# Kernel optimization log

Measured on AMD Instinct MI355X. Metric: run time of the kernel, lower is better.

## Reference

```python
import jax, jax.numpy as jnp
import numpy as np

NUM_HEADS = 64
D_K = 8  # n_wires of the quantum circuit


def setup_inputs() -> dict:
    key = jax.random.key(0)
    k1, k2, k3 = jax.random.split(key, 3)
    B, S, E = 8, 8192, NUM_HEADS * D_K
    x = jax.random.normal(k1, (B, S, E), dtype=jnp.float32)
    # trainable RX rotation angles, one per wire, shared across heads
    theta = jax.random.normal(k2, (D_K,), dtype=jnp.float32)
    # out_proj weight (torch nn.Linear stores [out_features, in_features]); bias=False
    W_out = jax.random.normal(k3, (E, E), dtype=jnp.float32) * 0.02
    return {"x": x, "theta": theta, "W_out": W_out}


def reference(x, theta, W_out):
    B, S, E = x.shape
    H, d = NUM_HEADS, D_K
    # Quantum circuit per (batch, seq, head) element:
    # RX(x_i) then RX(theta_i) on wire i from |0>, <Z_i> = cos(x_i + theta_i).
    xr = x.reshape(B, S, H, d)               # (B, S, H, d_k)
    A = jnp.cos(xr + theta)                  # broadcast theta over wires
    # torch stacks heads first -> (B, H, S, d), then .view(B, S, E) on the
    # contiguous buffer (a memory-layout reinterpretation, not a head-merge).
    A = jnp.transpose(A, (0, 2, 1, 3)).reshape(B, S, E)
    # out_proj: y = A @ W^T (no bias)
    return A @ W_out.T
```

## Files before the change

### kernel.cpp

```cpp
#include <hip/hip_runtime.h>
#include <hip/hip_bf16.h>

typedef __attribute__((ext_vector_type(8))) short short8;
typedef __attribute__((ext_vector_type(4))) float float4v;
typedef __attribute__((ext_vector_type(4))) unsigned int uint4v;
typedef __attribute__((ext_vector_type(2))) unsigned int uint2v;

#define SS 8192
#define EE 512
#define NKB 16
#define AP 520

__device__ __forceinline__ unsigned int f2bf1(float f) {
    unsigned int u = __builtin_bit_cast(unsigned int, f);
    return (u + 0x7fffu + ((u >> 16) & 1u)) >> 16;
}
__device__ __forceinline__ unsigned int pack2(float lo, float hi) {
    return f2bf1(lo) | (f2bf1(hi) << 16);
}

__global__ void w_prep(const float* __restrict__ W, unsigned short* __restrict__ Wws) {
    int idx = blockIdx.x * 256 + threadIdx.x;
    int n  = idx >> 7;
    int kg = idx & 127;
    int k  = kg * 4;
    float4v v = *(const float4v*)(W + (size_t)n * EE + k);
    int kb = k >> 5, kl = k & 31;
    unsigned short* dst = Wws + ((size_t)kb * (EE * 32) + (size_t)n * 32 + kl);
    uint2v pk = { pack2(v.x, v.y), pack2(v.z, v.w) };
    *(uint2v*)dst = pk;
}

__global__ __launch_bounds__(256, 2)
void qmha_fused5(const float* __restrict__ x, const float* __restrict__ theta,
                 const unsigned short* __restrict__ Wws, float* __restrict__ out)
{
    __shared__ __attribute__((aligned(16))) unsigned short A_lds[64 * AP];

    const int bx = blockIdx.x;
    const int b  = bx >> 7;
    const int sc = bx & 127;
    const int t = threadIdx.x, lane = t & 63, wid = t >> 6;
    const int fr = lane & 15, q = lane >> 4;

    const unsigned short* wbase = Wws + ((size_t)(wid * 128 + fr) * 32 + q * 8);

    short8 bA[8], bB[8];
    #pragma unroll
    for (int nt = 0; nt < 8; ++nt)
        bA[nt] = *(const short8*)(wbase + nt * 512);

    const float th0 = theta[0], th1 = theta[1], th2 = theta[2], th3 = theta[3];
    const float th4 = theta[4], th5 = theta[5], th6 = theta[6], th7 = theta[7];

    {
        const float* xb = x + ((size_t)b * SS + (size_t)sc * 64 + (size_t)wid * 16) * EE + lane * 8;
        unsigned short* aw = A_lds + lane * AP + wid * 128;
        #pragma unroll
        for (int it = 0; it < 16; ++it) {
            const float* px = xb + (size_t)it * EE;
            float4v v0 = *(const float4v*)(px);
            float4v v1 = *(const float4v*)(px + 4);
            float c0 = __cosf(v0.x + th0), c1 = __cosf(v0.y + th1);
            float c2 = __cosf(v0.z + th2), c3 = __cosf(v0.w + th3);
            float c4 = __cosf(v1.x + th4), c5 = __cosf(v1.y + th5);
            float c6 = __cosf(v1.z + th6), c7 = __cosf(v1.w + th7);
            uint4v pk = { pack2(c0,c1), pack2(c2,c3), pack2(c4,c5), pack2(c6,c7) };
            *(uint4v*)(aw + it * 8) = pk;
        }
    }

    __syncthreads();

    float4v acc[4][8];
    #pragma unroll
    for (int i = 0; i < 4; ++i)
        #pragma unroll
        for (int j = 0; j < 8; ++j)
            acc[i][j] = (float4v){0.f, 0.f, 0.f, 0.f};

    const int aoff = fr * AP + q * 8;

    #pragma unroll
    for (int kb = 0; kb < NKB; kb += 2) {
        {
            const unsigned short* wn = wbase + (size_t)(kb + 1) * (EE * 32);
            #pragma unroll
            for (int nt = 0; nt < 8; ++nt)
                bB[nt] = *(const short8*)(wn + nt * 512);
        }
        {
            short8 af[4];
            #pragma unroll
            for (int mt = 0; mt < 4; ++mt)
                af[mt] = *(const short8*)&A_lds[aoff + mt * 16 * AP + kb * 32];
            __builtin_amdgcn_s_setprio(1);
            #pragma unroll
            for (int nt = 0; nt < 8; ++nt)
                #pragma unroll
                for (int mt = 0; mt < 4; ++mt)
                    acc[mt][nt] = __builtin_amdgcn_mfma_f32_16x16x32_bf16(af[mt], bA[nt], acc[mt][nt], 0, 0, 0);
            __builtin_amdgcn_s_setprio(0);
        }
        if (kb + 2 < NKB) {
            const unsigned short* wn = wbase + (size_t)(kb + 2) * (EE * 32);
            #pragma unroll
            for (int nt = 0; nt < 8; ++nt)
                bA[nt] = *(const short8*)(wn + nt * 512);
        }
        {
            short8 af[4];
            #pragma unroll
            for (int mt = 0; mt < 4; ++mt)
                af[mt] = *(const short8*)&A_lds[aoff + mt * 16 * AP + (kb + 1) * 32];
            __builtin_amdgcn_s_setprio(1);
            #pragma unroll
            for (int nt = 0; nt < 8; ++nt)
                #pragma unroll
                for (int mt = 0; mt < 4; ++mt)
                    acc[mt][nt] = __builtin_amdgcn_mfma_f32_16x16x32_bf16(af[mt], bB[nt], acc[mt][nt], 0, 0, 0);
            __builtin_amdgcn_s_setprio(0);
        }
    }

    float* outb = out + (size_t)b * (SS * EE) + (size_t)sc * EE + wid * 128 + fr;
    #pragma unroll
    for (int mt = 0; mt < 4; ++mt) {
        #pragma unroll
        for (int r = 0; r < 4; ++r) {
            const int m = mt * 16 + q * 4 + r;
            float* po = outb + (size_t)m * (128 * EE);
            #pragma unroll
            for (int nt = 0; nt < 8; ++nt)
                po[nt * 16] = acc[mt][nt][r];
        }
    }
}

#define AS 520
#define WSF 40
#define HH 64
__global__ __launch_bounds__(256, 2)
void qmha_fused_fb(const float* __restrict__ x, const float* __restrict__ theta,
                   const float* __restrict__ W, float* __restrict__ out)
{
    __shared__ __attribute__((aligned(16))) unsigned short A_lds[HH * AS];
    __shared__ __attribute__((aligned(16))) unsigned short W_lds[128 * WSF];
    const int bx = blockIdx.x;
    const int ntile = (bx >> 3) & 3;
    const int p = ((bx >> 5) << 3) | (bx & 7);
    const int b = p >> 7;
    const int sc = p & 127;
    const int t = threadIdx.x, lane = t & 63, wid = t >> 6;
    const int wn = t >> 1, wk = (t & 1) * 16;
    const float* Wbase = W + (size_t)(ntile * 128 + wn) * EE + wk;
    float4v wv0 = *(const float4v*)(Wbase + 0);
    float4v wv1 = *(const float4v*)(Wbase + 4);
    float4v wv2 = *(const float4v*)(Wbase + 8);
    float4v wv3 = *(const float4v*)(Wbase + 12);
    const float th0 = theta[0], th1 = theta[1], th2 = theta[2], th3 = theta[3];
    const float th4 = theta[4], th5 = theta[5], th6 = theta[6], th7 = theta[7];
    {
        const float* xb = x + ((size_t)b * SS + (size_t)sc * 64) * EE + lane * 8;
        #pragma unroll
        for (int it = 0; it < 16; ++it) {
            const int s_loc = wid * 16 + it;
            const float* px = xb + (size_t)s_loc * EE;
            float4v v0 = *(const float4v*)(px);
            float4v v1 = *(const float4v*)(px + 4);
            float c0 = __cosf(v0.x + th0), c1 = __cosf(v0.y + th1);
            float c2 = __cosf(v0.z + th2), c3 = __cosf(v0.w + th3);
            float c4 = __cosf(v1.x + th4), c5 = __cosf(v1.y + th5);
            float c6 = __cosf(v1.z + th6), c7 = __cosf(v1.w + th7);
            uint4v pk = { pack2(c0,c1), pack2(c2,c3), pack2(c4,c5), pack2(c6,c7) };
            *(uint4v*)&A_lds[lane * AS + s_loc * 8] = pk;
        }
    }
    float4v acc[2][4];
    #pragma unroll
    for (int i = 0; i < 2; ++i)
        #pragma unroll
        for (int j = 0; j < 4; ++j)
            acc[i][j] = (float4v){0.f, 0.f, 0.f, 0.f};
    const int m0 = (wid >> 1) * 32, n0l = (wid & 1) * 64;
    const int fr = lane & 15, q = lane >> 4;
    const unsigned short* Arow0 = &A_lds[(m0 + fr) * AS + q * 8];
    const unsigned short* Arow1 = Arow0 + 16 * AS;
    const unsigned short* Wrow  = &W_lds[(n0l + fr) * WSF + q * 8];
    for (int kb = 0; kb < NKB; ++kb) {
        __syncthreads();
        {
            uint4v lo = { pack2(wv0.x, wv0.y), pack2(wv0.z, wv0.w),
                          pack2(wv1.x, wv1.y), pack2(wv1.z, wv1.w) };
            uint4v hi = { pack2(wv2.x, wv2.y), pack2(wv2.z, wv2.w),
                          pack2(wv3.x, wv3.y), pack2(wv3.z, wv3.w) };
            *(uint4v*)&W_lds[wn * WSF + wk]     = lo;
            *(uint4v*)&W_lds[wn * WSF + wk + 8] = hi;
        }
        if (kb < NKB - 1) {
            const float* Wn = Wbase + (size_t)(kb + 1) * 32;
            wv0 = *(const float4v*)(Wn + 0);
            wv1 = *(const float4v*)(Wn + 4);
            wv2 = *(const float4v*)(Wn + 8);
            wv3 = *(const float4v*)(Wn + 12);
        }
        __syncthreads();
        short8 a0 = *(const short8*)(Arow0 + kb * 32);
        short8 a1 = *(const short8*)(Arow1 + kb * 32);
        short8 b0 = *(const short8*)(Wrow + 0 * 16 * WSF);
        short8 b1 = *(const short8*)(Wrow + 1 * 16 * WSF);
        short8 b2 = *(const short8*)(Wrow + 2 * 16 * WSF);
        short8 b3 = *(const short8*)(Wrow + 3 * 16 * WSF);
        acc[0][0] = __builtin_amdgcn_mfma_f32_16x16x32_bf16(a0, b0, acc[0][0], 0, 0, 0);
        acc[0][1] = __builtin_amdgcn_mfma_f32_16x16x32_bf16(a0, b1, acc[0][1], 0, 0, 0);
        acc[0][2] = __builtin_amdgcn_mfma_f32_16x16x32_bf16(a0, b2, acc[0][2], 0, 0, 0);
        acc[0][3] = __builtin_amdgcn_mfma_f32_16x16x32_bf16(a0, b3, acc[0][3], 0, 0, 0);
        acc[1][0] = __builtin_amdgcn_mfma_f32_16x16x32_bf16(a1, b0, acc[1][0], 0, 0, 0);
        acc[1][1] = __builtin_amdgcn_mfma_f32_16x16x32_bf16(a1, b1, acc[1][1], 0, 0, 0);
        acc[1][2] = __builtin_amdgcn_mfma_f32_16x16x32_bf16(a1, b2, acc[1][2], 0, 0, 0);
        acc[1][3] = __builtin_amdgcn_mfma_f32_16x16x32_bf16(a1, b3, acc[1][3], 0, 0, 0);
    }
    const int colbase = ntile * 128 + n0l + fr;
    #pragma unroll
    for (int mt = 0; mt < 2; ++mt) {
        #pragma unroll
        for (int r = 0; r < 4; ++r) {
            const int hrow = m0 + mt * 16 + q * 4 + r;
            float* po = out + ((size_t)b * SS + (size_t)hrow * 128 + sc) * EE + colbase;
            po[0 * 16] = acc[mt][0][r];
            po[1 * 16] = acc[mt][1][r];
            po[2 * 16] = acc[mt][2][r];
            po[3 * 16] = acc[mt][3][r];
        }
    }
}

extern "C" void kernel_launch(void* const* d_in, const int* in_sizes, int n_in,
                              void* d_out, int out_size, void* d_ws, size_t ws_size,
                              hipStream_t stream) {
    const float* x     = (const float*)d_in[0];
    const float* theta = (const float*)d_in[1];
    const float* W     = (const float*)d_in[2];
    float* out         = (float*)d_out;

    if (ws_size >= (size_t)EE * EE * sizeof(unsigned short)) {
        unsigned short* Wws = (unsigned short*)d_ws;
        w_prep<<<dim3(256), dim3(256), 0, stream>>>(W, Wws);
        qmha_fused5<<<dim3(1024), dim3(256), 0, stream>>>(x, theta, Wws, out);
    } else {
        qmha_fused_fb<<<dim3(4096), dim3(256), 0, stream>>>(x, theta, W, out);
    }
}
```

Before: 257.7 us.

## Stage A-tile cosine production in chunks and overlap with MFMA loop

```diff
diff --git a/kernel.cpp b/kernel.cpp
--- a/kernel.cpp
+++ b/kernel.cpp
@@ -18,6 +18,8 @@
 __device__ __forceinline__ unsigned int pack2(float lo, float hi) {
     return f2bf1(lo) | (f2bf1(hi) << 16);
 }
+
+#define WAITL()  asm volatile("s_waitcnt lgkmcnt(0)" ::: "memory")
 
 __global__ void w_prep(const float* __restrict__ W, unsigned short* __restrict__ Wws) {
     int idx = blockIdx.x * 256 + threadIdx.x;
@@ -32,7 +34,7 @@
 }
 
 __global__ __launch_bounds__(256, 2)
-void qmha_fused5(const float* __restrict__ x, const float* __restrict__ theta,
+void qmha_fused6(const float* __restrict__ x, const float* __restrict__ theta,
                  const unsigned short* __restrict__ Wws, float* __restrict__ out)
 {
     __shared__ __attribute__((aligned(16))) unsigned short A_lds[64 * AP];
@@ -45,32 +47,55 @@
 
     const unsigned short* wbase = Wws + ((size_t)(wid * 128 + fr) * 32 + q * 8);
 
-    short8 bA[8], bB[8];
-    #pragma unroll
-    for (int nt = 0; nt < 8; ++nt)
-        bA[nt] = *(const short8*)(wbase + nt * 512);
+    const float* xq = x + ((size_t)b * SS + (size_t)sc * 64 + (size_t)wid * 4) * EE + lane * 8;
+    unsigned short* aw = A_lds + lane * AP + wid * 32;
 
     const float th0 = theta[0], th1 = theta[1], th2 = theta[2], th3 = theta[3];
     const float th4 = theta[4], th5 = theta[5], th6 = theta[6], th7 = theta[7];
 
-    {
-        const float* xb = x + ((size_t)b * SS + (size_t)sc * 64 + (size_t)wid * 16) * EE + lane * 8;
-        unsigned short* aw = A_lds + lane * AP + wid * 128;
-        #pragma unroll
-        for (int it = 0; it < 16; ++it) {
-            const float* px = xb + (size_t)it * EE;
-            float4v v0 = *(const float4v*)(px);
-            float4v v1 = *(const float4v*)(px + 4);
-            float c0 = __cosf(v0.x + th0), c1 = __cosf(v0.y + th1);
-            float c2 = __cosf(v0.z + th2), c3 = __cosf(v0.w + th3);
-            float c4 = __cosf(v1.x + th4), c5 = __cosf(v1.y + th5);
-            float c6 = __cosf(v1.z + th6), c7 = __cosf(v1.w + th7);
-            uint4v pk = { pack2(c0,c1), pack2(c2,c3), pack2(c4,c5), pack2(c6,c7) };
-            *(uint4v*)(aw + it * 8) = pk;
-        }
-    }
-
-    __syncthreads();
+    const int aoff = fr * AP + q * 8;
+
+    short8 bA[8], bB[8];
+    float4v xv0, xv1, yv0, yv1;
+
+#define BPF(KB, BUF) do { \
+    const unsigned short* _wn = wbase + (size_t)(KB) * (EE * 32); \
+    _Pragma("unroll") for (int _nt = 0; _nt < 8; ++_nt) \
+        BUF[_nt] = *(const short8*)(_wn + _nt * 512); \
+} while (0)
+
+#define AMM(KB, BUF) do { \
+    short8 _af[4]; \
+    _Pragma("unroll") for (int _mt = 0; _mt < 4; ++_mt) \
+        _af[_mt] = *(const short8*)&A_lds[aoff + _mt * 16 * AP + (KB) * 32]; \
+    __builtin_amdgcn_s_setprio(1); \
+    _Pragma("unroll") for (int _nt = 0; _nt < 8; ++_nt) \
+        _Pragma("unroll") for (int _mt = 0; _mt < 4; ++_mt) \
+            acc[_mt][_nt] = __builtin_amdgcn_mfma_f32_16x16x32_bf16(_af[_mt], BUF[_nt], acc[_mt][_nt], 0, 0, 0); \
+    __builtin_amdgcn_s_setprio(0); \
+} while (0)
+
+#define XISSV(V0, V1, Q, R) do { \
+    const float* _p = xq + (size_t)((Q) * 16 + (R)) * EE; \
+    V0 = *(const float4v*)_p; V1 = *(const float4v*)(_p + 4); \
+} while (0)
+
+#define XCONV(V0, V1, Q, R) do { \
+    float _c0 = __cosf((V0).x + th0), _c1 = __cosf((V0).y + th1); \
+    float _c2 = __cosf((V0).z + th2), _c3 = __cosf((V0).w + th3); \
+    float _c4 = __cosf((V1).x + th4), _c5 = __cosf((V1).y + th5); \
+    float _c6 = __cosf((V1).z + th6), _c7 = __cosf((V1).w + th7); \
+    uint4v _pk = { pack2(_c0,_c1), pack2(_c2,_c3), pack2(_c4,_c5), pack2(_c6,_c7) }; \
+    *(uint4v*)(aw + (Q) * 128 + (R) * 8) = _pk; \
+} while (0)
+
+    BPF(0, bA);
+    XISSV(xv0, xv1, 0, 0); XISSV(yv0, yv1, 0, 1);
+    XCONV(xv0, xv1, 0, 0); XISSV(xv0, xv1, 0, 2);
+    XCONV(yv0, yv1, 0, 1); XISSV(yv0, yv1, 0, 3);
+    XCONV(xv0, xv1, 0, 2); XCONV(yv0, yv1, 0, 3);
+    WAITL();
+    __builtin_amdgcn_s_barrier();
 
     float4v acc[4][8];
     #pragma unroll
@@ -79,49 +104,34 @@
         for (int j = 0; j < 8; ++j)
             acc[i][j] = (float4v){0.f, 0.f, 0.f, 0.f};
 
-    const int aoff = fr * AP + q * 8;
-
-    #pragma unroll
-    for (int kb = 0; kb < NKB; kb += 2) {
-        {
-            const unsigned short* wn = wbase + (size_t)(kb + 1) * (EE * 32);
-            #pragma unroll
-            for (int nt = 0; nt < 8; ++nt)
-                bB[nt] = *(const short8*)(wn + nt * 512);
-        }
-        {
-            short8 af[4];
-            #pragma unroll
-            for (int mt = 0; mt < 4; ++mt)
-                af[mt] = *(const short8*)&A_lds[aoff + mt * 16 * AP + kb * 32];
-            __builtin_amdgcn_s_setprio(1);
-            #pragma unroll
-            for (int nt = 0; nt < 8; ++nt)
-                #pragma unroll
-                for (int mt = 0; mt < 4; ++mt)
-                    acc[mt][nt] = __builtin_amdgcn_mfma_f32_16x16x32_bf16(af[mt], bA[nt], acc[mt][nt], 0, 0, 0);
-            __builtin_amdgcn_s_setprio(0);
-        }
-        if (kb + 2 < NKB) {
-            const unsigned short* wn = wbase + (size_t)(kb + 2) * (EE * 32);
-            #pragma unroll
-            for (int nt = 0; nt < 8; ++nt)
-                bA[nt] = *(const short8*)(wn + nt * 512);
-        }
-        {
-            short8 af[4];
-            #pragma unroll
-            for (int mt = 0; mt < 4; ++mt)
-                af[mt] = *(const short8*)&A_lds[aoff + mt * 16 * AP + (kb + 1) * 32];
-            __builtin_amdgcn_s_setprio(1);
-            #pragma unroll
-            for (int nt = 0; nt < 8; ++nt)
-                #pragma unroll
-                for (int mt = 0; mt < 4; ++mt)
-                    acc[mt][nt] = __builtin_amdgcn_mfma_f32_16x16x32_bf16(af[mt], bB[nt], acc[mt][nt], 0, 0, 0);
-            __builtin_amdgcn_s_setprio(0);
-        }
-    }
+    XISSV(xv0, xv1, 1, 0);                      BPF(1, bB); AMM(0, bA);
+    XCONV(xv0, xv1, 1, 0); XISSV(xv0, xv1, 1, 1); BPF(2, bA); AMM(1, bB);
+    XCONV(xv0, xv1, 1, 1); XISSV(xv0, xv1, 1, 2); BPF(3, bB); AMM(2, bA);
+    XCONV(xv0, xv1, 1, 2); XISSV(xv0, xv1, 1, 3); BPF(4, bA); AMM(3, bB);
+    XCONV(xv0, xv1, 1, 3);
+    WAITL();
+    __builtin_amdgcn_s_barrier();
+
+    XISSV(xv0, xv1, 2, 0);                      BPF(5, bB); AMM(4, bA);
+    XCONV(xv0, xv1, 2, 0); XISSV(xv0, xv1, 2, 1); BPF(6, bA); AMM(5, bB);
+    XCONV(xv0, xv1, 2, 1); XISSV(xv0, xv1, 2, 2); BPF(7, bB); AMM(6, bA);
+    XCONV(xv0, xv1, 2, 2); XISSV(xv0, xv1, 2, 3); BPF(8, bA); AMM(7, bB);
+    XCONV(xv0, xv1, 2, 3);
+    WAITL();
+    __builtin_amdgcn_s_barrier();
+
+    XISSV(xv0, xv1, 3, 0);                      BPF(9, bB);  AMM(8, bA);
+    XCONV(xv0, xv1, 3, 0); XISSV(xv0, xv1, 3, 1); BPF(10, bA); AMM(9, bB);
+    XCONV(xv0, xv1, 3, 1); XISSV(xv0, xv1, 3, 2); BPF(11, bB); AMM(10, bA);
+    XCONV(xv0, xv1, 3, 2); XISSV(xv0, xv1, 3, 3); BPF(12, bA); AMM(11, bB);
+    XCONV(xv0, xv1, 3, 3);
+    WAITL();
+    __builtin_amdgcn_s_barrier();
+
+    BPF(13, bB); AMM(12, bA);
+    BPF(14, bA); AMM(13, bB);
+    BPF(15, bB); AMM(14, bA);
+                 AMM(15, bB);
 
     float* outb = out + (size_t)b * (SS * EE) + (size_t)sc * EE + wid * 128 + fr;
     #pragma unroll
@@ -135,6 +145,10 @@
                 po[nt * 16] = acc[mt][nt][r];
         }
     }
+#undef BPF
+#undef AMM
+#undef XISSV
+#undef XCONV
 }
 
 #define AS 520
@@ -246,7 +260,7 @@
     if (ws_size >= (size_t)EE * EE * sizeof(unsigned short)) {
         unsigned short* Wws = (unsigned short*)d_ws;
         w_prep<<<dim3(256), dim3(256), 0, stream>>>(W, Wws);
-        qmha_fused5<<<dim3(1024), dim3(256), 0, stream>>>(x, theta, Wws, out);
+        qmha_fused6<<<dim3(1024), dim3(256), 0, stream>>>(x, theta, Wws, out);
     } else {
         qmha_fused_fb<<<dim3(4096), dim3(256), 0, stream>>>(x, theta, W, out);
     }
```

Result: faster. 251.7 us (-2.3%).

## Halve per-block M tile to 32 rows and raise occupancy to four blocks

Applied to the files above, without the earlier changes.

```diff
diff --git a/kernel.cpp b/kernel.cpp
--- a/kernel.cpp
+++ b/kernel.cpp
@@ -31,21 +31,22 @@
     *(uint2v*)dst = pk;
 }
 
-__global__ __launch_bounds__(256, 2)
-void qmha_fused5(const float* __restrict__ x, const float* __restrict__ theta,
+__global__ __launch_bounds__(256, 4)
+void qmha_fused8(const float* __restrict__ x, const float* __restrict__ theta,
                  const unsigned short* __restrict__ Wws, float* __restrict__ out)
 {
-    __shared__ __attribute__((aligned(16))) unsigned short A_lds[64 * AP];
+    __shared__ __attribute__((aligned(16))) unsigned short A_lds[32 * AP];
 
     const int bx = blockIdx.x;
-    const int b  = bx >> 7;
-    const int sc = bx & 127;
+    const int mh = bx & 1;
+    const int sc = (bx >> 1) & 127;
+    const int b  = bx >> 8;
     const int t = threadIdx.x, lane = t & 63, wid = t >> 6;
     const int fr = lane & 15, q = lane >> 4;
 
     const unsigned short* wbase = Wws + ((size_t)(wid * 128 + fr) * 32 + q * 8);
 
-    short8 bA[8], bB[8];
+    short8 bA[8];
     #pragma unroll
     for (int nt = 0; nt < 8; ++nt)
         bA[nt] = *(const short8*)(wbase + nt * 512);
@@ -54,11 +55,13 @@
     const float th4 = theta[4], th5 = theta[5], th6 = theta[6], th7 = theta[7];
 
     {
-        const float* xb = x + ((size_t)b * SS + (size_t)sc * 64 + (size_t)wid * 16) * EE + lane * 8;
-        unsigned short* aw = A_lds + lane * AP + wid * 128;
-        #pragma unroll
-        for (int it = 0; it < 16; ++it) {
-            const float* px = xb + (size_t)it * EE;
+        const int m = t & 31, g = t >> 5;
+        const float* xs = x + ((size_t)b * SS + (size_t)sc * 64 + (size_t)g * 8) * EE
+                          + mh * 256 + m * 8;
+        unsigned short* aw = A_lds + m * AP + g * 64;
+        #pragma unroll
+        for (int it = 0; it < 8; ++it) {
+            const float* px = xs + (size_t)it * EE;
             float4v v0 = *(const float4v*)(px);
             float4v v1 = *(const float4v*)(px + 4);
             float c0 = __cosf(v0.x + th0), c1 = __cosf(v0.y + th1);
@@ -72,9 +75,9 @@
 
     __syncthreads();
 
-    float4v acc[4][8];
-    #pragma unroll
-    for (int i = 0; i < 4; ++i)
+    float4v acc[2][8];
+    #pragma unroll
+    for (int i = 0; i < 2; ++i)
         #pragma unroll
         for (int j = 0; j < 8; ++j)
             acc[i][j] = (float4v){0.f, 0.f, 0.f, 0.f};
@@ -82,54 +85,32 @@
     const int aoff = fr * AP + q * 8;
 
     #pragma unroll
-    for (int kb = 0; kb < NKB; kb += 2) {
-        {
+    for (int kb = 0; kb < NKB; ++kb) {
+        short8 af0 = *(const short8*)&A_lds[aoff + kb * 32];
+        short8 af1 = *(const short8*)&A_lds[aoff + 16 * AP + kb * 32];
+        __builtin_amdgcn_s_setprio(1);
+        #pragma unroll
+        for (int nt = 0; nt < 8; ++nt) {
+            acc[0][nt] = __builtin_amdgcn_mfma_f32_16x16x32_bf16(af0, bA[nt], acc[0][nt], 0, 0, 0);
+            acc[1][nt] = __builtin_amdgcn_mfma_f32_16x16x32_bf16(af1, bA[nt], acc[1][nt], 0, 0, 0);
+        }
+        __builtin_amdgcn_s_setprio(0);
+        if (kb < NKB - 1) {
             const unsigned short* wn = wbase + (size_t)(kb + 1) * (EE * 32);
             #pragma unroll
             for (int nt = 0; nt < 8; ++nt)
-                bB[nt] = *(const short8*)(wn + nt * 512);
-        }
-        {
-            short8 af[4];
-            #pragma unroll
-            for (int mt = 0; mt < 4; ++mt)
-                af[mt] = *(const short8*)&A_lds[aoff + mt * 16 * AP + kb * 32];
-            __builtin_amdgcn_s_setprio(1);
-            #pragma unroll
-            for (int nt = 0; nt < 8; ++nt)
-                #pragma unroll
-                for (int mt = 0; mt < 4; ++mt)
-                    acc[mt][nt] = __builtin_amdgcn_mfma_f32_16x16x32_bf16(af[mt], bA[nt], acc[mt][nt], 0, 0, 0);
-            __builtin_amdgcn_s_setprio(0);
-        }
-        if (kb + 2 < NKB) {
-            const unsigned short* wn = wbase + (size_t)(kb + 2) * (EE * 32);
-            #pragma unroll
-            for (int nt = 0; nt < 8; ++nt)
                 bA[nt] = *(const short8*)(wn + nt * 512);
         }
-        {
-            short8 af[4];
-            #pragma unroll
-            for (int mt = 0; mt < 4; ++mt)
-                af[mt] = *(const short8*)&A_lds[aoff + mt * 16 * AP + (kb + 1) * 32];
-            __builtin_amdgcn_s_setprio(1);
-            #pragma unroll
-            for (int nt = 0; nt < 8; ++nt)
-                #pragma unroll
-                for (int mt = 0; mt < 4; ++mt)
-                    acc[mt][nt] = __builtin_amdgcn_mfma_f32_16x16x32_bf16(af[mt], bB[nt], acc[mt][nt], 0, 0, 0);
-            __builtin_amdgcn_s_setprio(0);
-        }
-    }
-
-    float* outb = out + (size_t)b * (SS * EE) + (size_t)sc * EE + wid * 128 + fr;
-    #pragma unroll
-    for (int mt = 0; mt < 4; ++mt) {
+    }
+
+    float* outb = out + (size_t)b * (SS * EE)
+                  + ((size_t)mh * 4096 + sc) * EE + wid * 128 + fr;
+    #pragma unroll
+    for (int mt = 0; mt < 2; ++mt) {
         #pragma unroll
         for (int r = 0; r < 4; ++r) {
-            const int m = mt * 16 + q * 4 + r;
-            float* po = outb + (size_t)m * (128 * EE);
+            const int mloc = mt * 16 + q * 4 + r;
+            float* po = outb + (size_t)mloc * (128 * EE);
             #pragma unroll
             for (int nt = 0; nt < 8; ++nt)
                 po[nt * 16] = acc[mt][nt][r];
@@ -246,7 +227,7 @@
     if (ws_size >= (size_t)EE * EE * sizeof(unsigned short)) {
         unsigned short* Wws = (unsigned short*)d_ws;
         w_prep<<<dim3(256), dim3(256), 0, stream>>>(W, Wws);
-        qmha_fused5<<<dim3(1024), dim3(256), 0, stream>>>(x, theta, Wws, out);
+        qmha_fused8<<<dim3(2048), dim3(256), 0, stream>>>(x, theta, Wws, out);
     } else {
         qmha_fused_fb<<<dim3(4096), dim3(256), 0, stream>>>(x, theta, W, out);
     }
```

Result: slower. 273.8 us (+6.3%).
